# Kernel tuning notes

Hardware: AMD Instinct MI355X
Metric: run time of the kernel (lower is better)

## Reference

```python
import jax, jax.numpy as jnp
import numpy as np

INPUT_SIZE = 1024
HEAD_SIZE = 64


def setup_inputs() -> dict:
    key = jax.random.key(0)
    kx, kk, kq, kv = jax.random.split(key, 4)
    B, T, C, H = 4, 4096, INPUT_SIZE, HEAD_SIZE
    x = jax.random.normal(kx, (B, T, C), dtype=jnp.float32)
    # nn.Linear(C, H, bias=False) weight is (H, C); we store transposed (C, H)
    # so that y = x @ W matches torch's x @ weight.T
    scale = 1.0 / np.sqrt(C)
    Wk = jax.random.uniform(kk, (C, H), dtype=jnp.float32, minval=-scale, maxval=scale)
    Wq = jax.random.uniform(kq, (C, H), dtype=jnp.float32, minval=-scale, maxval=scale)
    Wv = jax.random.uniform(kv, (C, H), dtype=jnp.float32, minval=-scale, maxval=scale)
    return {"x": x, "Wk": Wk, "Wq": Wq, "Wv": Wv}


def reference(x, Wk, Wq, Wv):
    B, T, C = x.shape
    k = x @ Wk  # (B, T, H)
    q = x @ Wq
    v = x @ Wv
    H = k.shape[-1]
    # scaled scores (B, T, T)
    wei = jnp.einsum('bth,bsh->bts', q, k) * (H ** -0.5)
    causal = jnp.tril(jnp.ones((T, T), dtype=bool))
    wei = jnp.where(causal, wei, -jnp.inf)
    wei = jax.nn.softmax(wei, axis=-1)
    out = jnp.einsum('bts,bsh->bth', wei, v)  # (B, T, H)
    return out
```

## Files before the change

### kernel.cpp

```cpp
#include <hip/hip_runtime.h>
#include <math.h>


#define BT   16384
#define TDIM 4096
#define CDIM 1024
#define HDIM 64
#define ACCW 68

typedef __attribute__((ext_vector_type(8))) short bf16x8;
typedef __attribute__((ext_vector_type(4))) float f32x4;
typedef __attribute__((ext_vector_type(8))) unsigned short us8;
typedef __attribute__((ext_vector_type(4))) unsigned short us4;

static __device__ __forceinline__ unsigned short f2bf(float f) {
    unsigned int u = __float_as_uint(f);
    u += 0x7fffu + ((u >> 16) & 1u);
    return (unsigned short)(u >> 16);
}

static __device__ __forceinline__ void pswap(unsigned &x, unsigned &y) {
    asm("v_permlane32_swap_b32 %0, %1" : "+v"(x), "+v"(y));
    asm("v_permlane16_swap_b32 %0, %1" : "+v"(x), "+v"(y));
}

__global__ __launch_bounds__(256) void wtrans_zero(
    const float* __restrict__ Wk, const float* __restrict__ Wq,
    const float* __restrict__ Wv, unsigned short* __restrict__ wtg,
    float* __restrict__ accp)
{
    int idx = blockIdx.x * 256 + threadIdx.x;
    int mat = idx >> 16;
    int rem = idx & 65535;
    int h = rem >> 10, c = rem & 1023;
    const float* W = (mat == 0) ? Wk : (mat == 1) ? Wq : Wv;
    wtg[idx] = f2bf(W[c * HDIM + h]);
    for (int i = idx; i < BT * ACCW; i += 196608) accp[i] = 0.f;
}

__global__ __launch_bounds__(512) void qkv_proj(
    const float* __restrict__ x, const unsigned short* __restrict__ wtg,
    unsigned short* __restrict__ kg, unsigned short* __restrict__ qg,
    unsigned short* __restrict__ vtg)
{
    __shared__ __align__(16) unsigned short xs[2][32][72];
    __shared__ __align__(16) unsigned short wts[2][192][72];
    const int t = threadIdx.x;
    const int lane = t & 63, wv = t >> 6, quad = lane >> 4, l16 = lane & 15;
    const int mt = wv >> 2;
    const int nq = wv & 3;
    const int row0 = blockIdx.x * 32;

    const int xr = t >> 4, xc4 = (t & 15) * 4;
    const int wn = t >> 3, wc8 = (t & 7) * 8;

    f32x4 acc3[3];
    #pragma unroll
    for (int i = 0; i < 3; i++) acc3[i] = (f32x4){0.f, 0.f, 0.f, 0.f};

    const size_t xrow = (size_t)(row0 + xr) * CDIM + xc4;

    float4 xv = *(const float4*)&x[xrow];
    us8 w0 = *(const us8*)&wtg[(size_t)(wn +   0) * CDIM + wc8];
    us8 w1 = *(const us8*)&wtg[(size_t)(wn +  64) * CDIM + wc8];
    us8 w2 = *(const us8*)&wtg[(size_t)(wn + 128) * CDIM + wc8];
    {
        us4 pk = { f2bf(xv.x), f2bf(xv.y), f2bf(xv.z), f2bf(xv.w) };
        *(us4*)&xs[0][xr][xc4] = pk;
        *(us8*)&wts[0][wn +   0][wc8] = w0;
        *(us8*)&wts[0][wn +  64][wc8] = w1;
        *(us8*)&wts[0][wn + 128][wc8] = w2;
    }
    xv = *(const float4*)&x[xrow + 64];
    w0 = *(const us8*)&wtg[(size_t)(wn +   0) * CDIM + 64 + wc8];
    w1 = *(const us8*)&wtg[(size_t)(wn +  64) * CDIM + 64 + wc8];
    w2 = *(const us8*)&wtg[(size_t)(wn + 128) * CDIM + 64 + wc8];
    __syncthreads();

    for (int it = 0; it < 16; it++) {
        const int buf = it & 1;
        if (it + 1 < 16) {
            us4 pk = { f2bf(xv.x), f2bf(xv.y), f2bf(xv.z), f2bf(xv.w) };
            *(us4*)&xs[buf ^ 1][xr][xc4] = pk;
            *(us8*)&wts[buf ^ 1][wn +   0][wc8] = w0;
            *(us8*)&wts[buf ^ 1][wn +  64][wc8] = w1;
            *(us8*)&wts[buf ^ 1][wn + 128][wc8] = w2;
            if (it + 2 < 16) {
                int nc = (it + 2) * 64;
                xv = *(const float4*)&x[xrow + nc];
                w0 = *(const us8*)&wtg[(size_t)(wn +   0) * CDIM + nc + wc8];
                w1 = *(const us8*)&wtg[(size_t)(wn +  64) * CDIM + nc + wc8];
                w2 = *(const us8*)&wtg[(size_t)(wn + 128) * CDIM + nc + wc8];
            }
        }
        bf16x8 a0 = *(const bf16x8*)&xs[buf][mt * 16 + l16][quad * 8];
        bf16x8 a1 = *(const bf16x8*)&xs[buf][mt * 16 + l16][32 + quad * 8];
        #pragma unroll
        for (int j = 0; j < 3; j++) {
            int nt = nq * 3 + j;
            bf16x8 b0 = *(const bf16x8*)&wts[buf][nt * 16 + l16][quad * 8];
            bf16x8 b1 = *(const bf16x8*)&wts[buf][nt * 16 + l16][32 + quad * 8];
            acc3[j] = __builtin_amdgcn_mfma_f32_16x16x32_bf16(a0, b0, acc3[j], 0, 0, 0);
            acc3[j] = __builtin_amdgcn_mfma_f32_16x16x32_bf16(a1, b1, acc3[j], 0, 0, 0);
        }
        __syncthreads();
    }

    const int mrow = row0 + mt * 16 + quad * 4;
    #pragma unroll
    for (int j = 0; j < 3; j++) {
        int nt = nq * 3 + j;
        int mat = nt >> 2;
        int col = (nt & 3) * 16 + l16;
        if (mat == 2) {
            int bb = mrow >> 12, tr = mrow & 4095;
            us4 pv = { f2bf(acc3[j][0]), f2bf(acc3[j][1]),
                       f2bf(acc3[j][2]), f2bf(acc3[j][3]) };
            *(us4*)&vtg[((size_t)(bb * HDIM + col) << 12) + tr] = pv;
        } else {
            float s = (mat == 1) ? 0.125f : 1.0f;
            unsigned short* dst = (mat == 0) ? kg : qg;
            #pragma unroll
            for (int reg = 0; reg < 4; reg++)
                dst[(size_t)(mrow + reg) * HDIM + col] = f2bf(acc3[j][reg] * s);
        }
    }
}

__global__ __launch_bounds__(256) void attn(
    const unsigned short* __restrict__ qg, const unsigned short* __restrict__ kg,
    const unsigned short* __restrict__ vtg, float* __restrict__ accp)
{
    __shared__ __align__(16) unsigned short Ks[2][64][72];
    __shared__ __align__(16) unsigned short Vt[2][64][72];

    const int t = threadIdx.x;
    const int lane = t & 63, wv = t >> 6, quad = lane >> 4, l16 = lane & 15;

    const int b = blockIdx.x / 160;
    const int s = blockIdx.x - b * 160;
    int qt, c;
    if (s < 16)      { qt = s;               c = 0; }
    else if (s < 48) { int u = s - 16; qt = 16 + (u >> 1); c = u & 1; }
    else if (s < 96) { int u = s - 48; int q3 = u / 3; qt = 32 + q3; c = u - 3 * q3; }
    else             { int u = s - 96; qt = 48 + (u >> 2); c = u & 3; }

    const size_t bbase = (size_t)b * TDIM;
    const int Q0 = qt * 64;
    const int kt0 = c * 16;
    const int kt1 = (kt0 + 15 < qt) ? kt0 + 15 : qt;

    const int qrow = Q0 + wv * 16 + l16;
    const bf16x8 qa0 = *(const bf16x8*)&qg[(bbase + qrow) * HDIM + quad * 8];
    const bf16x8 qa1 = *(const bf16x8*)&qg[(bbase + qrow) * HDIM + 32 + quad * 8];

    const short onev = (l16 == 0) ? (short)0x3F80 : (short)0;
    const bf16x8 ones = { onev, onev, onev, onev, onev, onev, onev, onev };

    f32x4 O[5];
    #pragma unroll
    for (int i = 0; i < 5; i++) O[i] = (f32x4){0.f, 0.f, 0.f, 0.f};

    const int fr = t >> 3, fc = (t & 7) * 8;

    us8 kr0 = *(const us8*)&kg[(bbase + kt0 * 64 + fr) * HDIM + fc];
    us8 kr1 = *(const us8*)&kg[(bbase + kt0 * 64 + fr + 32) * HDIM + fc];
    us8 vr0 = *(const us8*)&vtg[((size_t)(b * HDIM + fr) << 12) + kt0 * 64 + fc];
    us8 vr1 = *(const us8*)&vtg[((size_t)(b * HDIM + fr + 32) << 12) + kt0 * 64 + fc];
    *(us8*)&Ks[0][fr][fc] = kr0;
    *(us8*)&Ks[0][fr + 32][fc] = kr1;
    *(us8*)&Vt[0][fr][fc] = vr0;
    *(us8*)&Vt[0][fr + 32][fc] = vr1;
    if (kt0 < kt1) {
        int kn = kt0 + 1;
        kr0 = *(const us8*)&kg[(bbase + kn * 64 + fr) * HDIM + fc];
        kr1 = *(const us8*)&kg[(bbase + kn * 64 + fr + 32) * HDIM + fc];
        vr0 = *(const us8*)&vtg[((size_t)(b * HDIM + fr) << 12) + kn * 64 + fc];
        vr1 = *(const us8*)&vtg[((size_t)(b * HDIM + fr + 32) << 12) + kn * 64 + fc];
    }
    __syncthreads();

    const int qloc = wv * 16 + l16;
    int buf = 0;
    for (int kt = kt0; kt <= kt1; kt++) {
        f32x4 sT[4];
        #pragma unroll
        for (int st = 0; st < 4; st++) {
            bf16x8 kb0 = *(const bf16x8*)&Ks[buf][st * 16 + l16][quad * 8];
            bf16x8 kb1 = *(const bf16x8*)&Ks[buf][st * 16 + l16][32 + quad * 8];
            f32x4 z = (f32x4){0.f, 0.f, 0.f, 0.f};
            z = __builtin_amdgcn_mfma_f32_16x16x32_bf16(kb0, qa0, z, 0, 0, 0);
            z = __builtin_amdgcn_mfma_f32_16x16x32_bf16(kb1, qa1, z, 0, 0, 0);
            sT[st] = z;
        }

        if (kt < kt1) {
            *(us8*)&Ks[buf ^ 1][fr][fc] = kr0;
            *(us8*)&Ks[buf ^ 1][fr + 32][fc] = kr1;
            *(us8*)&Vt[buf ^ 1][fr][fc] = vr0;
            *(us8*)&Vt[buf ^ 1][fr + 32][fc] = vr1;
            if (kt + 1 < kt1) {
                int kn = kt + 2;
                kr0 = *(const us8*)&kg[(bbase + kn * 64 + fr) * HDIM + fc];
                kr1 = *(const us8*)&kg[(bbase + kn * 64 + fr + 32) * HDIM + fc];
                vr0 = *(const us8*)&vtg[((size_t)(b * HDIM + fr) << 12) + kn * 64 + fc];
                vr1 = *(const us8*)&vtg[((size_t)(b * HDIM + fr + 32) << 12) + kn * 64 + fc];
            }
        }

        float p[4][4];
        if (kt == qt) {
            #pragma unroll
            for (int st = 0; st < 4; st++)
                #pragma unroll
                for (int r = 0; r < 4; r++) {
                    int kkloc = st * 16 + quad * 4 + r;
                    p[st][r] = (kkloc > qloc) ? 0.f : __expf(sT[st][r]);
                }
        } else {
            #pragma unroll
            for (int st = 0; st < 4; st++)
                #pragma unroll
                for (int r = 0; r < 4; r++)
                    p[st][r] = __expf(sT[st][r]);
        }

        unsigned cpk[4][2];
        #pragma unroll
        for (int st = 0; st < 4; st++) {
            asm("v_cvt_pk_bf16_f32 %0, %1, %2"
                : "=v"(cpk[st][0]) : "v"(p[st][0]), "v"(p[st][1]));
            asm("v_cvt_pk_bf16_f32 %0, %1, %2"
                : "=v"(cpk[st][1]) : "v"(p[st][2]), "v"(p[st][3]));
        }
        union { unsigned u[4]; bf16x8 v; } pa0u, pa1u;
        {
            unsigned a0 = cpk[0][0], b0 = cpk[1][0]; pswap(a0, b0);
            unsigned a1 = cpk[0][1], b1 = cpk[1][1]; pswap(a1, b1);
            pa0u.u[0] = a0; pa0u.u[1] = a1; pa0u.u[2] = b0; pa0u.u[3] = b1;
            unsigned a2 = cpk[2][0], b2 = cpk[3][0]; pswap(a2, b2);
            unsigned a3 = cpk[2][1], b3 = cpk[3][1]; pswap(a3, b3);
            pa1u.u[0] = a2; pa1u.u[1] = a3; pa1u.u[2] = b2; pa1u.u[3] = b3;
        }
        const bf16x8 pa0 = pa0u.v, pa1 = pa1u.v;

        #pragma unroll
        for (int nt = 0; nt < 4; nt++) {
            bf16x8 vb0 = *(const bf16x8*)&Vt[buf][nt * 16 + l16][quad * 8];
            bf16x8 vb1 = *(const bf16x8*)&Vt[buf][nt * 16 + l16][32 + quad * 8];
            O[nt] = __builtin_amdgcn_mfma_f32_16x16x32_bf16(pa0, vb0, O[nt], 0, 0, 0);
            O[nt] = __builtin_amdgcn_mfma_f32_16x16x32_bf16(pa1, vb1, O[nt], 0, 0, 0);
        }
        O[4] = __builtin_amdgcn_mfma_f32_16x16x32_bf16(pa0, ones, O[4], 0, 0, 0);
        O[4] = __builtin_amdgcn_mfma_f32_16x16x32_bf16(pa1, ones, O[4], 0, 0, 0);

        __syncthreads();
        buf ^= 1;
    }

    const int grow = (b << 12) + Q0 + wv * 16 + quad * 4;
    #pragma unroll
    for (int nt = 0; nt < 4; nt++)
        #pragma unroll
        for (int r = 0; r < 4; r++)
            atomicAdd(&accp[(size_t)(grow + r) * ACCW + nt * 16 + l16], O[nt][r]);
    if (l16 == 0) {
        #pragma unroll
        for (int r = 0; r < 4; r++)
            atomicAdd(&accp[(size_t)(grow + r) * ACCW + 64], O[4][r]);
    }
}

__global__ __launch_bounds__(256) void normalize(
    const float* __restrict__ accp, float* __restrict__ out)
{
    int idx = blockIdx.x * 256 + threadIdx.x;
    int row = idx >> 4, c4 = (idx & 15) * 4;
    float inv = 1.f / accp[(size_t)row * ACCW + 64];
    float4 o = *(const float4*)&accp[(size_t)row * ACCW + c4];
    float4 res = make_float4(o.x * inv, o.y * inv, o.z * inv, o.w * inv);
    *(float4*)&out[(size_t)row * HDIM + c4] = res;
}

extern "C" void kernel_launch(void* const* d_in, const int* in_sizes, int n_in,
                              void* d_out, int out_size, void* d_ws, size_t ws_size,
                              hipStream_t stream) {
    const float* x  = (const float*)d_in[0];
    const float* Wk = (const float*)d_in[1];
    const float* Wq = (const float*)d_in[2];
    const float* Wv = (const float*)d_in[3];
    float* out = (float*)d_out;

    unsigned short* wtg = (unsigned short*)d_ws;
    unsigned short* kg  = wtg + 196608;
    unsigned short* qg  = kg + (size_t)BT * HDIM;
    unsigned short* vtg = qg + (size_t)BT * HDIM;
    float* accp = (float*)(vtg + (size_t)4 * HDIM * TDIM);

    wtrans_zero<<<768, 256, 0, stream>>>(Wk, Wq, Wv, wtg, accp);
    qkv_proj<<<BT / 32, 512, 0, stream>>>(x, wtg, kg, qg, vtg);
    attn<<<4 * 160, 256, 0, stream>>>(qg, kg, vtg, accp);
    normalize<<<BT * HDIM / (4 * 256), 256, 0, stream>>>(accp, out);
}
```

Baseline: 143.5 us.

## Split causal attention into finer key chunks with per-slot partial slabs

Result: no change. 141.9 us (-1.1%).

```diff
diff --git a/kernel.cpp b/kernel.cpp
--- a/kernel.cpp
+++ b/kernel.cpp
@@ -7,6 +7,7 @@
 #define CDIM 1024
 #define HDIM 64
 #define ACCW 68
+#define NSLOT 288
 
 typedef __attribute__((ext_vector_type(8))) short bf16x8;
 typedef __attribute__((ext_vector_type(4))) float f32x4;
@@ -24,10 +25,9 @@
     asm("v_permlane16_swap_b32 %0, %1" : "+v"(x), "+v"(y));
 }
 
-__global__ __launch_bounds__(256) void wtrans_zero(
+__global__ __launch_bounds__(256) void wtrans(
     const float* __restrict__ Wk, const float* __restrict__ Wq,
-    const float* __restrict__ Wv, unsigned short* __restrict__ wtg,
-    float* __restrict__ accp)
+    const float* __restrict__ Wv, unsigned short* __restrict__ wtg)
 {
     int idx = blockIdx.x * 256 + threadIdx.x;
     int mat = idx >> 16;
@@ -35,7 +35,6 @@
     int h = rem >> 10, c = rem & 1023;
     const float* W = (mat == 0) ? Wk : (mat == 1) ? Wq : Wv;
     wtg[idx] = f2bf(W[c * HDIM + h]);
-    for (int i = idx; i < BT * ACCW; i += 196608) accp[i] = 0.f;
 }
 
 __global__ __launch_bounds__(512) void qkv_proj(
@@ -129,7 +128,7 @@
 
 __global__ __launch_bounds__(256) void attn(
     const unsigned short* __restrict__ qg, const unsigned short* __restrict__ kg,
-    const unsigned short* __restrict__ vtg, float* __restrict__ accp)
+    const unsigned short* __restrict__ vtg, float* __restrict__ slabs)
 {
     __shared__ __align__(16) unsigned short Ks[2][64][72];
     __shared__ __align__(16) unsigned short Vt[2][64][72];
@@ -137,18 +136,25 @@
     const int t = threadIdx.x;
     const int lane = t & 63, wv = t >> 6, quad = lane >> 4, l16 = lane & 15;
 
-    const int b = blockIdx.x / 160;
-    const int s = blockIdx.x - b * 160;
-    int qt, c;
-    if (s < 16)      { qt = s;               c = 0; }
-    else if (s < 48) { int u = s - 16; qt = 16 + (u >> 1); c = u & 1; }
-    else if (s < 96) { int u = s - 48; int q3 = u / 3; qt = 32 + q3; c = u - 3 * q3; }
-    else             { int u = s - 96; qt = 48 + (u >> 2); c = u & 3; }
+    const int b = blockIdx.x / NSLOT;
+    const int s = blockIdx.x - b * NSLOT;
+    int a;
+    if      (s < 8)   a = 0;
+    else if (s < 24)  a = 1;
+    else if (s < 48)  a = 2;
+    else if (s < 80)  a = 3;
+    else if (s < 120) a = 4;
+    else if (s < 168) a = 5;
+    else if (s < 224) a = 6;
+    else              a = 7;
+    const int u  = s - 4 * a * (a + 1);
+    const int qt = a * 8 + u / (a + 1);
+    const int c  = u % (a + 1);
 
     const size_t bbase = (size_t)b * TDIM;
     const int Q0 = qt * 64;
-    const int kt0 = c * 16;
-    const int kt1 = (kt0 + 15 < qt) ? kt0 + 15 : qt;
+    const int kt0 = c * 8;
+    const int kt1 = (kt0 + 7 < qt) ? kt0 + 7 : qt;
 
     const int qrow = Q0 + wv * 16 + l16;
     const bf16x8 qa0 = *(const bf16x8*)&qg[(bbase + qrow) * HDIM + quad * 8];
@@ -258,28 +264,41 @@
         buf ^= 1;
     }
 
-    const int grow = (b << 12) + Q0 + wv * 16 + quad * 4;
+    float* slab = slabs + (size_t)(b * NSLOT + s) * 64 * ACCW;
+    const int rl = wv * 16 + quad * 4;
     #pragma unroll
     for (int nt = 0; nt < 4; nt++)
         #pragma unroll
         for (int r = 0; r < 4; r++)
-            atomicAdd(&accp[(size_t)(grow + r) * ACCW + nt * 16 + l16], O[nt][r]);
+            slab[(size_t)(rl + r) * ACCW + nt * 16 + l16] = O[nt][r];
     if (l16 == 0) {
         #pragma unroll
         for (int r = 0; r < 4; r++)
-            atomicAdd(&accp[(size_t)(grow + r) * ACCW + 64], O[4][r]);
-    }
-}
-
-__global__ __launch_bounds__(256) void normalize(
-    const float* __restrict__ accp, float* __restrict__ out)
+            slab[(size_t)(rl + r) * ACCW + 64] = O[4][r];
+    }
+}
+
+__global__ __launch_bounds__(256) void reduce_norm(
+    const float* __restrict__ slabs, float* __restrict__ out)
 {
     int idx = blockIdx.x * 256 + threadIdx.x;
     int row = idx >> 4, c4 = (idx & 15) * 4;
-    float inv = 1.f / accp[(size_t)row * ACCW + 64];
-    float4 o = *(const float4*)&accp[(size_t)row * ACCW + c4];
-    float4 res = make_float4(o.x * inv, o.y * inv, o.z * inv, o.w * inv);
-    *(float4*)&out[(size_t)row * HDIM + c4] = res;
+    int b = row >> 12, qt = (row >> 6) & 63, r64 = row & 63;
+    int a = qt >> 3, nc = a + 1;
+    int base = 4 * a * (a + 1) + (qt & 7) * nc;
+
+    const float* sl = slabs + ((size_t)(b * NSLOT + base) * 64 + r64) * ACCW;
+    float4 o = make_float4(0.f, 0.f, 0.f, 0.f);
+    float l = 0.f;
+    for (int i = 0; i < nc; i++) {
+        float4 v = *(const float4*)&sl[c4];
+        o.x += v.x; o.y += v.y; o.z += v.z; o.w += v.w;
+        l += sl[64];
+        sl += (size_t)64 * ACCW;
+    }
+    float inv = 1.f / l;
+    *(float4*)&out[(size_t)row * HDIM + c4] =
+        make_float4(o.x * inv, o.y * inv, o.z * inv, o.w * inv);
 }
 
 extern "C" void kernel_launch(void* const* d_in, const int* in_sizes, int n_in,
@@ -295,10 +314,10 @@
     unsigned short* kg  = wtg + 196608;
     unsigned short* qg  = kg + (size_t)BT * HDIM;
     unsigned short* vtg = qg + (size_t)BT * HDIM;
-    float* accp = (float*)(vtg + (size_t)4 * HDIM * TDIM);
-
-    wtrans_zero<<<768, 256, 0, stream>>>(Wk, Wq, Wv, wtg, accp);
+    float* slabs = (float*)(vtg + (size_t)4 * HDIM * TDIM);
+
+    wtrans<<<768, 256, 0, stream>>>(Wk, Wq, Wv, wtg);
     qkv_proj<<<BT / 32, 512, 0, stream>>>(x, wtg, kg, qg, vtg);
-    attn<<<4 * 160, 256, 0, stream>>>(qg, kg, vtg, accp);
-    normalize<<<BT * HDIM / (4 * 256), 256, 0, stream>>>(accp, out);
-}
+    attn<<<4 * NSLOT, 256, 0, stream>>>(qg, kg, vtg, slabs);
+    reduce_norm<<<BT * HDIM / (4 * 256), 256, 0, stream>>>(slabs, out);
+}
```
